# Kernel tuning notes

Measured on AMD Instinct MI355X. Metric: run time of the kernel, lower is better.

## Reference

```python
import jax, jax.numpy as jnp
from jax import lax
import numpy as np

T, B, D, H = 1024, 512, 128, 128  # time steps, batch, input dim, hidden size


def setup_inputs() -> dict:
    key = jax.random.key(0)
    ks = jax.random.split(key, 8)
    s_fc = 1.0 / np.sqrt(D)
    s_gru = 1.0 / np.sqrt(H)
    return {
        "x": jax.random.normal(ks[0], (T, B, D), dtype=jnp.float32),
        "W1": jax.random.uniform(ks[1], (128, D), jnp.float32, -s_fc, s_fc),
        "b1": jax.random.uniform(ks[2], (128,), jnp.float32, -s_fc, s_fc),
        "W_ih": jax.random.uniform(ks[3], (3 * H, 128), jnp.float32, -s_gru, s_gru),
        "W_hh": jax.random.uniform(ks[4], (3 * H, H), jnp.float32, -s_gru, s_gru),
        "b_ih": jax.random.uniform(ks[5], (3 * H,), jnp.float32, -s_gru, s_gru),
        "b_hh": jax.random.uniform(ks[6], (3 * H,), jnp.float32, -s_gru, s_gru),
    }


def reference(x, W1, b1, W_ih, W_hh, b_ih, b_hh):
    # fc1 applied to every step (batched once over T*B for efficiency)
    feats = jnp.einsum('tbd,hd->tbh', x, W1) + b1  # [T, B, 128]

    hidden = W_hh.shape[1]

    def step(h, f):
        # PyTorch GRUCell gate math
        gi = f @ W_ih.T + b_ih          # [B, 3H]
        gh = h @ W_hh.T + b_hh          # [B, 3H]
        i_r, i_z, i_n = jnp.split(gi, 3, axis=-1)
        h_r, h_z, h_n = jnp.split(gh, 3, axis=-1)
        r = jax.nn.sigmoid(i_r + h_r)
        z = jax.nn.sigmoid(i_z + h_z)
        n = jnp.tanh(i_n + r * h_n)
        h_new = (1.0 - z) * n + z * h
        return h_new, None

    # first call gru(feats) passes no hidden -> zeros initial state
    h0 = jnp.zeros((x.shape[1], hidden), dtype=x.dtype)
    h_final, _ = lax.scan(step, h0, feats)
    return h_final  # [B, H]
```

## Files before the change

### kernel.cpp

```cpp
#include <hip/hip_runtime.h>
#include <hip/hip_bf16.h>

#define T_STEPS 1024
#define BATCH   512
#define DIM     128
#define G3      384
#define NCHUNK  (T_STEPS/8)

typedef __attribute__((ext_vector_type(8))) short bf16x8;
typedef __attribute__((ext_vector_type(4))) float f32x4;

#define LOG2E  1.44269504f
#define LOG2E2 2.88539008f

#define HSTRIDE 160

__device__ __forceinline__ short f2bf(float f) {
  unsigned u = __builtin_bit_cast(unsigned, f);
  u += 0x7FFFu + ((u >> 16) & 1u);
  return (short)(u >> 16);
}

__device__ __forceinline__ void block_sync_lds() {
  asm volatile("s_waitcnt lgkmcnt(0)\n\ts_barrier" ::: "memory");
}

__global__ void prep_kernel(const float* __restrict__ W1, const float* __restrict__ b1,
                            const float* __restrict__ W_ih, const float* __restrict__ W_hh,
                            const float* __restrict__ b_ih, const float* __restrict__ b_hh,
                            short* __restrict__ wc_bf, short* __restrict__ whh_bf,
                            float* __restrict__ bc, float* __restrict__ bhh_s) {
  const int g = blockIdx.x;
  const int d = threadIdx.x;
  const float sg = (g < 256) ? -LOG2E : LOG2E2;
  float acc = 0.f;
  #pragma unroll 4
  for (int k = 0; k < 128; ++k)
    acc = fmaf(W_ih[g * 128 + k], W1[k * 128 + d], acc);
  wc_bf[g * 128 + d]  = f2bf(acc * sg);
  whh_bf[g * 128 + d] = f2bf(W_hh[g * 128 + d] * sg);

  __shared__ float red[128];
  red[d] = W_ih[g * 128 + d] * b1[d];
  __syncthreads();
  #pragma unroll
  for (int s = 64; s > 0; s >>= 1) {
    if (d < s) red[d] += red[d + s];
    __syncthreads();
  }
  if (d == 0) {
    bc[g]    = (red[0] + b_ih[g]) * sg;
    bhh_s[g] = b_hh[g] * sg;
  }
}

__global__ __launch_bounds__(512, 2) void gru_kernel(
    const float* __restrict__ x,
    const float* __restrict__ bhh_s,
    const short* __restrict__ wc_bf,
    const short* __restrict__ whh_bf,
    const float* __restrict__ bc,
    float* __restrict__ out)
{
  const int tid = threadIdx.x;
  const int w   = tid >> 6;
  const int l   = tid & 63;
  const int q   = l >> 4;
  const int c   = l & 15;
  const int b0  = blockIdx.x * 2;

  __shared__ f32x4 gi4[2][16][128];
  __shared__ short hbuf[2][2][HSTRIDE];

  const f32x4 zero4 = {0.f, 0.f, 0.f, 0.f};

  if (w < 4) {
    const int half = q & 1;
    const int ch   = q >> 1;
    const int colX = w * 32 + (half << 4) + c;

    bf16x8 Bh[3][2][4];
    #pragma unroll
    for (int g = 0; g < 3; ++g)
      #pragma unroll
      for (int Tt = 0; Tt < 2; ++Tt)
        #pragma unroll
        for (int kt = 0; kt < 4; ++kt)
          Bh[g][Tt][kt] = *(const bf16x8*)(whh_bf +
              (g * 128 + w * 32 + Tt * 16 + c) * 128 + kt * 32 + q * 8);
    const float bhn = bhh_s[256 + colX];
    const f32x4 bhn4 = {bhn, 0.f, 0.f, 0.f};

    ((short*)hbuf)[tid] = 0;
    if (tid < 2 * HSTRIDE - 256) ((short*)hbuf)[256 + tid] = 0;
    float hp = 0.f;
    __syncthreads();

    const short* hb0 = &hbuf[0][c >> 3][q * 8];
    const short* hb1 = &hbuf[1][c >> 3][q * 8];

    __builtin_amdgcn_s_setprio(1);
    for (int cc = 0; cc < NCHUNK; ++cc) {
      const f32x4* gp = &gi4[cc & 1][ch][colX];
      f32x4 gcur = gp[0];
      #pragma unroll
      for (int s = 0; s < 8; ++s) {
        const short* hb = (s & 1) ? hb1 : hb0;
        bf16x8 Ah[4];
        #pragma unroll
        for (int kt = 0; kt < 4; ++kt)
          Ah[kt] = *(const bf16x8*)(hb + kt * 32);
        f32x4 gnext = gp[2 * ((s + 1) & 7) * 128];
        const f32x4 gz = {gcur[1], 0.f, 0.f, 0.f};

        f32x4 r0A = __builtin_amdgcn_mfma_f32_16x16x32_bf16(Ah[0], Bh[0][0][0], gcur, 0, 0, 0);
        f32x4 r1A = __builtin_amdgcn_mfma_f32_16x16x32_bf16(Ah[0], Bh[0][1][0], gcur, 0, 0, 0);
        f32x4 r0B = __builtin_amdgcn_mfma_f32_16x16x32_bf16(Ah[2], Bh[0][0][2], zero4, 0, 0, 0);
        f32x4 r1B = __builtin_amdgcn_mfma_f32_16x16x32_bf16(Ah[2], Bh[0][1][2], zero4, 0, 0, 0);
        f32x4 n0A = __builtin_amdgcn_mfma_f32_16x16x32_bf16(Ah[0], Bh[2][0][0], bhn4, 0, 0, 0);
        f32x4 n1A = __builtin_amdgcn_mfma_f32_16x16x32_bf16(Ah[0], Bh[2][1][0], bhn4, 0, 0, 0);
        f32x4 n0B = __builtin_amdgcn_mfma_f32_16x16x32_bf16(Ah[2], Bh[2][0][2], zero4, 0, 0, 0);
        f32x4 n1B = __builtin_amdgcn_mfma_f32_16x16x32_bf16(Ah[2], Bh[2][1][2], zero4, 0, 0, 0);
        f32x4 z0A = __builtin_amdgcn_mfma_f32_16x16x32_bf16(Ah[0], Bh[1][0][0], gz, 0, 0, 0);
        f32x4 z1A = __builtin_amdgcn_mfma_f32_16x16x32_bf16(Ah[0], Bh[1][1][0], gz, 0, 0, 0);
        f32x4 z0B = __builtin_amdgcn_mfma_f32_16x16x32_bf16(Ah[2], Bh[1][0][2], zero4, 0, 0, 0);
        f32x4 z1B = __builtin_amdgcn_mfma_f32_16x16x32_bf16(Ah[2], Bh[1][1][2], zero4, 0, 0, 0);

        r0A = __builtin_amdgcn_mfma_f32_16x16x32_bf16(Ah[1], Bh[0][0][1], r0A, 0, 0, 0);
        r1A = __builtin_amdgcn_mfma_f32_16x16x32_bf16(Ah[1], Bh[0][1][1], r1A, 0, 0, 0);
        r0B = __builtin_amdgcn_mfma_f32_16x16x32_bf16(Ah[3], Bh[0][0][3], r0B, 0, 0, 0);
        r1B = __builtin_amdgcn_mfma_f32_16x16x32_bf16(Ah[3], Bh[0][1][3], r1B, 0, 0, 0);
        n0A = __builtin_amdgcn_mfma_f32_16x16x32_bf16(Ah[1], Bh[2][0][1], n0A, 0, 0, 0);
        n1A = __builtin_amdgcn_mfma_f32_16x16x32_bf16(Ah[1], Bh[2][1][1], n1A, 0, 0, 0);
        n0B = __builtin_amdgcn_mfma_f32_16x16x32_bf16(Ah[3], Bh[2][0][3], n0B, 0, 0, 0);
        n1B = __builtin_amdgcn_mfma_f32_16x16x32_bf16(Ah[3], Bh[2][1][3], n1B, 0, 0, 0);
        z0A = __builtin_amdgcn_mfma_f32_16x16x32_bf16(Ah[1], Bh[1][0][1], z0A, 0, 0, 0);
        z1A = __builtin_amdgcn_mfma_f32_16x16x32_bf16(Ah[1], Bh[1][1][1], z1A, 0, 0, 0);
        z0B = __builtin_amdgcn_mfma_f32_16x16x32_bf16(Ah[3], Bh[1][0][3], z0B, 0, 0, 0);
        z1B = __builtin_amdgcn_mfma_f32_16x16x32_bf16(Ah[3], Bh[1][1][3], z1B, 0, 0, 0);

        const float arg_r = half ? (r1A[0] + r1B[0]) : (r0A[0] + r0B[0]);
        const float rg = __builtin_amdgcn_rcpf(1.f + __builtin_amdgcn_exp2f(arg_r));
        const float ghn_b = half ? (n1A[0] + n1B[0]) : (n0A[0] + n0B[0]);
        const float nv = fmaf(rg, ghn_b, gcur[2]);
        const float e  = __builtin_amdgcn_exp2f(nv);
        const float nn = 1.f - 2.f * __builtin_amdgcn_rcpf(e + 1.f);
        const float arg_z = half ? (z1A[0] + z1B[0]) : (z0A[0] + z0B[0]);
        const float zg = __builtin_amdgcn_rcpf(1.f + __builtin_amdgcn_exp2f(arg_z));
        const float h  = fmaf(zg, hp - nn, nn);
        hp = h;
        hbuf[(s & 1) ^ 1][ch][colX] = f2bf(h);
        gcur = gnext;
        block_sync_lds();
      }
    }
    __builtin_amdgcn_s_setprio(0);
    out[(size_t)(b0 + ch) * DIM + colX] = hp;
  } else {
    const int w4 = w - 4;
    const int jg0 = w4 * 32 + c, jg1 = jg0 + 16;
    bf16x8 Bc[3][2][4];
    #pragma unroll
    for (int g = 0; g < 3; ++g)
      #pragma unroll
      for (int Tt = 0; Tt < 2; ++Tt)
        #pragma unroll
        for (int kt = 0; kt < 4; ++kt)
          Bc[g][Tt][kt] = *(const bf16x8*)(wc_bf +
              (g * 128 + w4 * 32 + Tt * 16 + c) * 128 + kt * 32 + q * 8);
    const float fr0 = bc[jg0]       + bhh_s[jg0];
    const float fz0 = bc[128 + jg0] + bhh_s[128 + jg0];
    const float fn0 = bc[256 + jg0];
    const float fr1 = bc[jg1]       + bhh_s[jg1];
    const float fz1 = bc[128 + jg1] + bhh_s[128 + jg1];
    const float fn1 = bc[256 + jg1];

    const int trel = c >> 1, chn = c & 1;
    f32x4 xv[8];

    {
      const float* xb = x + ((size_t)trel * BATCH + (b0 + chn)) * DIM + q * 8;
      f32x4 xt[8];
      #pragma unroll
      for (int kt = 0; kt < 4; ++kt) {
        xt[2 * kt]     = *(const f32x4*)(xb + kt * 32);
        xt[2 * kt + 1] = *(const f32x4*)(xb + kt * 32 + 4);
      }
      bf16x8 Ax[4];
      #pragma unroll
      for (int kt = 0; kt < 4; ++kt) {
        const f32x4 v0 = xt[2 * kt], v1 = xt[2 * kt + 1];
        bf16x8 a;
        a[0] = f2bf(v0[0]); a[1] = f2bf(v0[1]); a[2] = f2bf(v0[2]); a[3] = f2bf(v0[3]);
        a[4] = f2bf(v1[0]); a[5] = f2bf(v1[1]); a[6] = f2bf(v1[2]); a[7] = f2bf(v1[3]);
        Ax[kt] = a;
      }
      f32x4 ga[2][3];
      #pragma unroll
      for (int g = 0; g < 3; ++g) {
        ga[0][g] = __builtin_amdgcn_mfma_f32_16x16x32_bf16(Ax[0], Bc[g][0][0], zero4, 0, 0, 0);
        ga[1][g] = __builtin_amdgcn_mfma_f32_16x16x32_bf16(Ax[0], Bc[g][1][0], zero4, 0, 0, 0);
      }
      #pragma unroll
      for (int kt = 1; kt < 4; ++kt)
        #pragma unroll
        for (int g = 0; g < 3; ++g) {
          ga[0][g] = __builtin_amdgcn_mfma_f32_16x16x32_bf16(Ax[kt], Bc[g][0][kt], ga[0][g], 0, 0, 0);
          ga[1][g] = __builtin_amdgcn_mfma_f32_16x16x32_bf16(Ax[kt], Bc[g][1][kt], ga[1][g], 0, 0, 0);
        }
      #pragma unroll
      for (int r = 0; r < 4; ++r) {
        f32x4 vA = {ga[0][0][r] + fr0, ga[0][1][r] + fz0, ga[0][2][r] + fn0, 0.f};
        f32x4 vB = {ga[1][0][r] + fr1, ga[1][1][r] + fz1, ga[1][2][r] + fn1, 0.f};
        gi4[0][4 * q + r][jg0] = vA;
        gi4[0][4 * q + r][jg1] = vB;
      }
      const float* xb1 = x + ((size_t)(8 + trel) * BATCH + (b0 + chn)) * DIM + q * 8;
      #pragma unroll
      for (int kt = 0; kt < 4; ++kt) {
        xv[2 * kt]     = *(const f32x4*)(xb1 + kt * 32);
        xv[2 * kt + 1] = *(const f32x4*)(xb1 + kt * 32 + 4);
      }
    }
    __syncthreads();

    for (int cc = 0; cc < NCHUNK; ++cc) {
      const int tc = cc + 1;
      bf16x8 Ax[4];
      f32x4 ga[2][3];
      #pragma unroll
      for (int s = 0; s < 8; ++s) {
        if (tc < NCHUNK) {
          if (s == 0 || s == 1 || s == 3 || s == 4) {
            const int ck = (s < 2) ? s : s - 1;
            const f32x4 v0 = xv[2 * ck], v1 = xv[2 * ck + 1];
            bf16x8 a;
            a[0] = f2bf(v0[0]); a[1] = f2bf(v0[1]); a[2] = f2bf(v0[2]); a[3] = f2bf(v0[3]);
            a[4] = f2bf(v1[0]); a[5] = f2bf(v1[1]); a[6] = f2bf(v1[2]); a[7] = f2bf(v1[3]);
            Ax[ck] = a;
          }
          if (s >= 1 && s <= 6) {
            #pragma unroll
            for (int uu = 0; uu < 2; ++uu) {
              const int u = 2 * (s - 1) + uu;
              const int kt = u / 3, g = u % 3;
              if (kt == 0) {
                ga[0][g] = __builtin_amdgcn_mfma_f32_16x16x32_bf16(Ax[0], Bc[g][0][0], zero4, 0, 0, 0);
                ga[1][g] = __builtin_amdgcn_mfma_f32_16x16x32_bf16(Ax[0], Bc[g][1][0], zero4, 0, 0, 0);
              } else {
                ga[0][g] = __builtin_amdgcn_mfma_f32_16x16x32_bf16(Ax[kt], Bc[g][0][kt], ga[0][g], 0, 0, 0);
                ga[1][g] = __builtin_amdgcn_mfma_f32_16x16x32_bf16(Ax[kt], Bc[g][1][kt], ga[1][g], 0, 0, 0);
              }
            }
            if (s == 5 && tc + 1 < NCHUNK) {
              const float* xb = x + ((size_t)((tc + 1) * 8 + trel) * BATCH + (b0 + chn)) * DIM + q * 8;
              #pragma unroll
              for (int kt = 0; kt < 4; ++kt) {
                xv[2 * kt]     = *(const f32x4*)(xb + kt * 32);
                xv[2 * kt + 1] = *(const f32x4*)(xb + kt * 32 + 4);
              }
            }
          } else if (s == 7) {
            const int nbuf = tc & 1;
            #pragma unroll
            for (int r = 0; r < 4; ++r) {
              f32x4 vA = {ga[0][0][r] + fr0, ga[0][1][r] + fz0, ga[0][2][r] + fn0, 0.f};
              f32x4 vB = {ga[1][0][r] + fr1, ga[1][1][r] + fz1, ga[1][2][r] + fn1, 0.f};
              gi4[nbuf][4 * q + r][jg0] = vA;
              gi4[nbuf][4 * q + r][jg1] = vB;
            }
          }
        }
        block_sync_lds();
      }
    }
  }
}

extern "C" void kernel_launch(void* const* d_in, const int* in_sizes, int n_in,
                              void* d_out, int out_size, void* d_ws, size_t ws_size,
                              hipStream_t stream) {
  const float* x    = (const float*)d_in[0];
  const float* W1   = (const float*)d_in[1];
  const float* b1   = (const float*)d_in[2];
  const float* W_ih = (const float*)d_in[3];
  const float* W_hh = (const float*)d_in[4];
  const float* b_ih = (const float*)d_in[5];
  const float* b_hh = (const float*)d_in[6];
  float* out = (float*)d_out;

  char* ws = (char*)d_ws;
  short* wc_bf  = (short*)(ws);
  short* whh_bf = (short*)(ws + 98304);
  float* bc     = (float*)(ws + 196608);
  float* bhh_s  = (float*)(ws + 198144);

  prep_kernel<<<dim3(G3), dim3(128), 0, stream>>>(W1, b1, W_ih, W_hh, b_ih, b_hh,
                                                  wc_bf, whh_bf, bc, bhh_s);
  gru_kernel<<<dim3(BATCH / 2), dim3(512), 0, stream>>>(x, bhh_s, wc_bf, whh_bf, bc, out);
}
```

Before: 670.2 us.

## Quantize recurrent weights and hidden state to int8 for i8 MFMA

Quantizes W_hh per row to int8 with a stored dequant scale, and the hidden state to int8 (scale 127). The recurrent matmul then uses mfma_i32_16x16x64_i8, halving the MFMA count per step on the serial critical path. Biases and dequant are applied in the scalar epilogue instead of through the accumulator inputs. This trades numerical accuracy, since the hidden state gets only about 8 bits over 1024 steps, and may fail tolerance.

```diff
diff --git a/kernel.cpp b/kernel.cpp
--- a/kernel.cpp
+++ b/kernel.cpp
@@ -9,11 +9,10 @@
 
 typedef __attribute__((ext_vector_type(8))) short bf16x8;
 typedef __attribute__((ext_vector_type(4))) float f32x4;
+typedef __attribute__((ext_vector_type(4))) int   i32x4;
 
 #define LOG2E  1.44269504f
 #define LOG2E2 2.88539008f
-
-#define HSTRIDE 160
 
 __device__ __forceinline__ short f2bf(float f) {
   unsigned u = __builtin_bit_cast(unsigned, f);
@@ -28,8 +27,9 @@
 __global__ void prep_kernel(const float* __restrict__ W1, const float* __restrict__ b1,
                             const float* __restrict__ W_ih, const float* __restrict__ W_hh,
                             const float* __restrict__ b_ih, const float* __restrict__ b_hh,
-                            short* __restrict__ wc_bf, short* __restrict__ whh_bf,
-                            float* __restrict__ bc, float* __restrict__ bhh_s) {
+                            short* __restrict__ wc_bf, char* __restrict__ whh_i8,
+                            float* __restrict__ bc, float* __restrict__ bhh_s,
+                            float* __restrict__ dqs) {
   const int g = blockIdx.x;
   const int d = threadIdx.x;
   const float sg = (g < 256) ? -LOG2E : LOG2E2;
@@ -37,10 +37,24 @@
   #pragma unroll 4
   for (int k = 0; k < 128; ++k)
     acc = fmaf(W_ih[g * 128 + k], W1[k * 128 + d], acc);
-  wc_bf[g * 128 + d]  = f2bf(acc * sg);
-  whh_bf[g * 128 + d] = f2bf(W_hh[g * 128 + d] * sg);
+  wc_bf[g * 128 + d] = f2bf(acc * sg);
 
   __shared__ float red[128];
+  __shared__ float srow_sh;
+
+  red[d] = fabsf(W_hh[g * 128 + d]);
+  __syncthreads();
+  #pragma unroll
+  for (int s = 64; s > 0; s >>= 1) {
+    if (d < s) red[d] = fmaxf(red[d], red[d + s]);
+    __syncthreads();
+  }
+  if (d == 0) srow_sh = fmaxf(red[0], 1e-30f);
+  __syncthreads();
+  const float qs = 127.f / srow_sh;
+  whh_i8[g * 128 + d] = (char)(int)rintf(W_hh[g * 128 + d] * qs);
+  __syncthreads();
+
   red[d] = W_ih[g * 128 + d] * b1[d];
   __syncthreads();
   #pragma unroll
@@ -51,6 +65,7 @@
   if (d == 0) {
     bc[g]    = (red[0] + b_ih[g]) * sg;
     bhh_s[g] = b_hh[g] * sg;
+    dqs[g]   = sg * srow_sh / 16129.f;
   }
 }
 
@@ -58,8 +73,9 @@
     const float* __restrict__ x,
     const float* __restrict__ bhh_s,
     const short* __restrict__ wc_bf,
-    const short* __restrict__ whh_bf,
+    const char*  __restrict__ whh_i8,
     const float* __restrict__ bc,
+    const float* __restrict__ dqs,
     float* __restrict__ out)
 {
   const int tid = threadIdx.x;
@@ -70,7 +86,7 @@
   const int b0  = blockIdx.x * 2;
 
   __shared__ f32x4 gi4[2][16][128];
-  __shared__ short hbuf[2][2][HSTRIDE];
+  __shared__ __align__(16) char hbuf8[2][2][192];
 
   const f32x4 zero4 = {0.f, 0.f, 0.f, 0.f};
 
@@ -79,25 +95,28 @@
     const int ch   = q >> 1;
     const int colX = w * 32 + (half << 4) + c;
 
-    bf16x8 Bh[3][2][4];
+    i32x4 Bi[3][2][2];
     #pragma unroll
     for (int g = 0; g < 3; ++g)
       #pragma unroll
       for (int Tt = 0; Tt < 2; ++Tt)
         #pragma unroll
-        for (int kt = 0; kt < 4; ++kt)
-          Bh[g][Tt][kt] = *(const bf16x8*)(whh_bf +
-              (g * 128 + w * 32 + Tt * 16 + c) * 128 + kt * 32 + q * 8);
-    const float bhn = bhh_s[256 + colX];
-    const f32x4 bhn4 = {bhn, 0.f, 0.f, 0.f};
-
-    ((short*)hbuf)[tid] = 0;
-    if (tid < 2 * HSTRIDE - 256) ((short*)hbuf)[256 + tid] = 0;
+        for (int kt = 0; kt < 2; ++kt)
+          Bi[g][Tt][kt] = *(const i32x4*)(whh_i8 +
+              (g * 128 + w * 32 + Tt * 16 + c) * 128 + kt * 64 + q * 16);
+    const float dq_r = dqs[colX];
+    const float dq_z = dqs[128 + colX];
+    const float dq_n = dqs[256 + colX];
+    const float bhn  = bhh_s[256 + colX];
+
+    if (tid < 192) ((int*)hbuf8)[tid] = 0;
     float hp = 0.f;
     __syncthreads();
 
-    const short* hb0 = &hbuf[0][c >> 3][q * 8];
-    const short* hb1 = &hbuf[1][c >> 3][q * 8];
+    const char* hb0 = &hbuf8[0][c >> 3][q * 16];
+    const char* hb1 = &hbuf8[1][c >> 3][q * 16];
+
+    const i32x4 zeroI = {0, 0, 0, 0};
 
     __builtin_amdgcn_s_setprio(1);
     for (int cc = 0; cc < NCHUNK; ++cc) {
@@ -105,51 +124,38 @@
       f32x4 gcur = gp[0];
       #pragma unroll
       for (int s = 0; s < 8; ++s) {
-        const short* hb = (s & 1) ? hb1 : hb0;
-        bf16x8 Ah[4];
-        #pragma unroll
-        for (int kt = 0; kt < 4; ++kt)
-          Ah[kt] = *(const bf16x8*)(hb + kt * 32);
+        const char* hb = (s & 1) ? hb1 : hb0;
+        i32x4 a0 = *(const i32x4*)(hb);
+        i32x4 a1 = *(const i32x4*)(hb + 64);
         f32x4 gnext = gp[2 * ((s + 1) & 7) * 128];
-        const f32x4 gz = {gcur[1], 0.f, 0.f, 0.f};
-
-        f32x4 r0A = __builtin_amdgcn_mfma_f32_16x16x32_bf16(Ah[0], Bh[0][0][0], gcur, 0, 0, 0);
-        f32x4 r1A = __builtin_amdgcn_mfma_f32_16x16x32_bf16(Ah[0], Bh[0][1][0], gcur, 0, 0, 0);
-        f32x4 r0B = __builtin_amdgcn_mfma_f32_16x16x32_bf16(Ah[2], Bh[0][0][2], zero4, 0, 0, 0);
-        f32x4 r1B = __builtin_amdgcn_mfma_f32_16x16x32_bf16(Ah[2], Bh[0][1][2], zero4, 0, 0, 0);
-        f32x4 n0A = __builtin_amdgcn_mfma_f32_16x16x32_bf16(Ah[0], Bh[2][0][0], bhn4, 0, 0, 0);
-        f32x4 n1A = __builtin_amdgcn_mfma_f32_16x16x32_bf16(Ah[0], Bh[2][1][0], bhn4, 0, 0, 0);
-        f32x4 n0B = __builtin_amdgcn_mfma_f32_16x16x32_bf16(Ah[2], Bh[2][0][2], zero4, 0, 0, 0);
-        f32x4 n1B = __builtin_amdgcn_mfma_f32_16x16x32_bf16(Ah[2], Bh[2][1][2], zero4, 0, 0, 0);
-        f32x4 z0A = __builtin_amdgcn_mfma_f32_16x16x32_bf16(Ah[0], Bh[1][0][0], gz, 0, 0, 0);
-        f32x4 z1A = __builtin_amdgcn_mfma_f32_16x16x32_bf16(Ah[0], Bh[1][1][0], gz, 0, 0, 0);
-        f32x4 z0B = __builtin_amdgcn_mfma_f32_16x16x32_bf16(Ah[2], Bh[1][0][2], zero4, 0, 0, 0);
-        f32x4 z1B = __builtin_amdgcn_mfma_f32_16x16x32_bf16(Ah[2], Bh[1][1][2], zero4, 0, 0, 0);
-
-        r0A = __builtin_amdgcn_mfma_f32_16x16x32_bf16(Ah[1], Bh[0][0][1], r0A, 0, 0, 0);
-        r1A = __builtin_amdgcn_mfma_f32_16x16x32_bf16(Ah[1], Bh[0][1][1], r1A, 0, 0, 0);
-        r0B = __builtin_amdgcn_mfma_f32_16x16x32_bf16(Ah[3], Bh[0][0][3], r0B, 0, 0, 0);
-        r1B = __builtin_amdgcn_mfma_f32_16x16x32_bf16(Ah[3], Bh[0][1][3], r1B, 0, 0, 0);
-        n0A = __builtin_amdgcn_mfma_f32_16x16x32_bf16(Ah[1], Bh[2][0][1], n0A, 0, 0, 0);
-        n1A = __builtin_amdgcn_mfma_f32_16x16x32_bf16(Ah[1], Bh[2][1][1], n1A, 0, 0, 0);
-        n0B = __builtin_amdgcn_mfma_f32_16x16x32_bf16(Ah[3], Bh[2][0][3], n0B, 0, 0, 0);
-        n1B = __builtin_amdgcn_mfma_f32_16x16x32_bf16(Ah[3], Bh[2][1][3], n1B, 0, 0, 0);
-        z0A = __builtin_amdgcn_mfma_f32_16x16x32_bf16(Ah[1], Bh[1][0][1], z0A, 0, 0, 0);
-        z1A = __builtin_amdgcn_mfma_f32_16x16x32_bf16(Ah[1], Bh[1][1][1], z1A, 0, 0, 0);
-        z0B = __builtin_amdgcn_mfma_f32_16x16x32_bf16(Ah[3], Bh[1][0][3], z0B, 0, 0, 0);
-        z1B = __builtin_amdgcn_mfma_f32_16x16x32_bf16(Ah[3], Bh[1][1][3], z1B, 0, 0, 0);
-
-        const float arg_r = half ? (r1A[0] + r1B[0]) : (r0A[0] + r0B[0]);
+
+        i32x4 r0 = __builtin_amdgcn_mfma_i32_16x16x64_i8(a0, Bi[0][0][0], zeroI, 0, 0, 0);
+        i32x4 r1 = __builtin_amdgcn_mfma_i32_16x16x64_i8(a0, Bi[0][1][0], zeroI, 0, 0, 0);
+        i32x4 n0 = __builtin_amdgcn_mfma_i32_16x16x64_i8(a0, Bi[2][0][0], zeroI, 0, 0, 0);
+        i32x4 n1 = __builtin_amdgcn_mfma_i32_16x16x64_i8(a0, Bi[2][1][0], zeroI, 0, 0, 0);
+        i32x4 z0 = __builtin_amdgcn_mfma_i32_16x16x64_i8(a0, Bi[1][0][0], zeroI, 0, 0, 0);
+        i32x4 z1 = __builtin_amdgcn_mfma_i32_16x16x64_i8(a0, Bi[1][1][0], zeroI, 0, 0, 0);
+        r0 = __builtin_amdgcn_mfma_i32_16x16x64_i8(a1, Bi[0][0][1], r0, 0, 0, 0);
+        r1 = __builtin_amdgcn_mfma_i32_16x16x64_i8(a1, Bi[0][1][1], r1, 0, 0, 0);
+        n0 = __builtin_amdgcn_mfma_i32_16x16x64_i8(a1, Bi[2][0][1], n0, 0, 0, 0);
+        n1 = __builtin_amdgcn_mfma_i32_16x16x64_i8(a1, Bi[2][1][1], n1, 0, 0, 0);
+        z0 = __builtin_amdgcn_mfma_i32_16x16x64_i8(a1, Bi[1][0][1], z0, 0, 0, 0);
+        z1 = __builtin_amdgcn_mfma_i32_16x16x64_i8(a1, Bi[1][1][1], z1, 0, 0, 0);
+
+        const float fr = (float)(half ? r1[0] : r0[0]);
+        const float arg_r = fmaf(fr, dq_r, gcur[0]);
         const float rg = __builtin_amdgcn_rcpf(1.f + __builtin_amdgcn_exp2f(arg_r));
-        const float ghn_b = half ? (n1A[0] + n1B[0]) : (n0A[0] + n0B[0]);
-        const float nv = fmaf(rg, ghn_b, gcur[2]);
+        const float fn = (float)(half ? n1[0] : n0[0]);
+        const float tn = fmaf(fn, dq_n, bhn);
+        const float nv = fmaf(rg, tn, gcur[2]);
         const float e  = __builtin_amdgcn_exp2f(nv);
         const float nn = 1.f - 2.f * __builtin_amdgcn_rcpf(e + 1.f);
-        const float arg_z = half ? (z1A[0] + z1B[0]) : (z0A[0] + z0B[0]);
+        const float fz = (float)(half ? z1[0] : z0[0]);
+        const float arg_z = fmaf(fz, dq_z, gcur[1]);
         const float zg = __builtin_amdgcn_rcpf(1.f + __builtin_amdgcn_exp2f(arg_z));
         const float h  = fmaf(zg, hp - nn, nn);
         hp = h;
-        hbuf[(s & 1) ^ 1][ch][colX] = f2bf(h);
+        hbuf8[(s & 1) ^ 1][ch][colX] = (char)(int)rintf(h * 127.f);
         gcur = gnext;
         block_sync_lds();
       }
@@ -291,11 +297,12 @@
 
   char* ws = (char*)d_ws;
   short* wc_bf  = (short*)(ws);
-  short* whh_bf = (short*)(ws + 98304);
-  float* bc     = (float*)(ws + 196608);
-  float* bhh_s  = (float*)(ws + 198144);
+  char*  whh_i8 = (char*) (ws + 98304);
+  float* bc     = (float*)(ws + 147456);
+  float* bhh_s  = (float*)(ws + 148992);
+  float* dqs    = (float*)(ws + 150528);
 
   prep_kernel<<<dim3(G3), dim3(128), 0, stream>>>(W1, b1, W_ih, W_hh, b_ih, b_hh,
-                                                  wc_bf, whh_bf, bc, bhh_s);
-  gru_kernel<<<dim3(BATCH / 2), dim3(512), 0, stream>>>(x, bhh_s, wc_bf, whh_bf, bc, out);
-}
+                                                  wc_bf, whh_i8, bc, bhh_s, dqs);
+  gru_kernel<<<dim3(BATCH / 2), dim3(512), 0, stream>>>(x, bhh_s, wc_bf, whh_i8, bc, dqs, out);
+}
```

Result: faster. 615.6 us (-8.2%).
